# Optimization experiments

Hardware: AMD Instinct MI355X
Metric: run time of the kernel (lower is better)

Reference implementation:

```python
import jax, jax.numpy as jnp
import numpy as np

B, S, E, H = 2, 2048, 1024, 16
D = E // H  # head_dim = 64

def setup_inputs() -> dict:
    key = jax.random.key(0)
    ks = jax.random.split(key, 11)
    s = 1.0 / np.sqrt(E)
    inp = {
        'query': jax.random.normal(ks[0], (B, S, E), jnp.float32),
        'key':   jax.random.normal(ks[1], (B, S, E), jnp.float32),
        'value': jax.random.normal(ks[2], (B, S, E), jnp.float32),
        'Wq': jax.random.uniform(ks[3], (E, E), jnp.float32, -s, s),
        'bq': jax.random.uniform(ks[4], (E,), jnp.float32, -s, s),
        'Wk': jax.random.uniform(ks[5], (E, E), jnp.float32, -s, s),
        'bk': jax.random.uniform(ks[6], (E,), jnp.float32, -s, s),
        'Wv': jax.random.uniform(ks[7], (E, E), jnp.float32, -s, s),
        'bv': jax.random.uniform(ks[8], (E,), jnp.float32, -s, s),
        'Wo': jax.random.uniform(ks[9], (E, E), jnp.float32, -s, s),
        'bo': jax.random.uniform(ks[10], (E,), jnp.float32, -s, s),
    }
    return inp

def reference(query, key, value, Wq, bq, Wk, bk, Wv, bv, Wo, bo):
    # project and split heads: [B,S,E] -> [B,H,S,D]
    def proj(x, W, b):
        y = jnp.einsum('bse,fe->bsf', x, W) + b  # torch Linear: x @ W.T + b
        return y.reshape(B, S, H, D).transpose(0, 2, 1, 3)
    q = proj(query, Wq, bq)
    k = proj(key, Wk, bk)
    v = proj(value, Wv, bv)
    scores = jnp.einsum('bhqd,bhkd->bhqk', q, k) / jnp.sqrt(jnp.float32(D))
    attn = jax.nn.softmax(scores, axis=-1)
    out = jnp.einsum('bhqk,bhkd->bhqd', attn, v)  # [B,H,S,D]
    out = out.transpose(0, 2, 1, 3).reshape(B, S, E)
    return jnp.einsum('bse,fe->bsf', out, Wo) + bo
```

## Files before the change

### kernel.cpp

```cpp
#include <hip/hip_runtime.h>

#define B_ 2
#define S_ 2048
#define E_ 1024
#define H_ 16
#define D_ 64
#define M_ (B_*S_)
#define K_ E_

typedef __attribute__((ext_vector_type(8))) short  short8;
typedef __attribute__((ext_vector_type(4))) float  f32x4;
typedef __attribute__((ext_vector_type(8))) unsigned short u16x8;
typedef __attribute__((ext_vector_type(4))) unsigned short u16x4;
typedef __attribute__((ext_vector_type(4))) unsigned int   u32x4;

#define QSCALE 0.18033688011112042f

#if __has_builtin(__builtin_amdgcn_exp2f)
#define EXP2F(x) __builtin_amdgcn_exp2f(x)
#else
#define EXP2F(x) exp2f(x)
#endif

__device__ __forceinline__ unsigned short f2bf(float f) {
    unsigned u = __float_as_uint(f);
    u += 0x7fffu + ((u >> 16) & 1u);
    return (unsigned short)(u >> 16);
}

__device__ __forceinline__ void gl_lds16(const ushort* g, ushort* l) {
    __builtin_amdgcn_global_load_lds((const __attribute__((address_space(1))) void*)g,
                                     (__attribute__((address_space(3))) void*)l,
                                     16, 0, 0);
}

#define FL_SYNC(N) do {                                                   \
    asm volatile("s_waitcnt vmcnt(" #N ")" ::: "memory");                 \
    __builtin_amdgcn_s_barrier();                                         \
    asm volatile("" ::: "memory");                                        \
} while (0)

#define WAITL0_BAR() do {                                                 \
    asm volatile("s_waitcnt lgkmcnt(0)" ::: "memory");                    \
    __builtin_amdgcn_s_barrier();                                         \
    asm volatile("" ::: "memory");                                        \
} while (0)

__global__ __launch_bounds__(256)
void cvt_all(const float* __restrict__ q, const float* __restrict__ k,
             const float* __restrict__ v, const float* __restrict__ wq,
             const float* __restrict__ wk, const float* __restrict__ wv,
             const float* __restrict__ wo, ushort* __restrict__ dst)
{
    const int bid = blockIdx.x;
    const float* src;
    size_t dof;
    int local;
    if (bid < 6144) {
        const int t = bid >> 11;
        src = (t == 0) ? q : (t == 1) ? k : v;
        dof = (size_t)t * 4194304u;
        local = bid & 2047;
    } else {
        const int r = bid - 6144;
        const int t = r >> 9;
        src = (t == 0) ? wq : (t == 1) ? wk : (t == 2) ? wv : wo;
        dof = 12582912u + (size_t)t * 1048576u;
        local = r & 511;
    }
    const size_t idx = (size_t)local * 2048 + threadIdx.x * 8;
    const float4 a = *(const float4*)(src + idx);
    const float4 b = *(const float4*)(src + idx + 4);
    u16x8 o;
    o[0] = f2bf(a.x); o[1] = f2bf(a.y); o[2] = f2bf(a.z); o[3] = f2bf(a.w);
    o[4] = f2bf(b.x); o[5] = f2bf(b.y); o[6] = f2bf(b.z); o[7] = f2bf(b.w);
    *(u16x8*)(dst + dof + idx) = o;
}

template<int SWAP>
__device__ __forceinline__ void qkv_core(const ushort* __restrict__ X,
                                         const ushort* __restrict__ W,
                                         int m0, int n0,
                                         f32x4 acc[8][4], ushort* sh)
{
    const int tid  = threadIdx.x;
    const int lane = tid & 63;
    const int w    = tid >> 6;
    const int wm   = w & 1;
    const int wn   = w >> 1;
    const int l15  = lane & 15, quad = lane >> 4;

    const int srow = lane >> 3, schunk = lane & 7;
    const int scol = (schunk ^ srow) * 8;
    const ushort* pa[4]; const ushort* pb[4]; int loff[4];
    #pragma unroll
    for (int i = 0; i < 4; ++i) {
        const int row = (w * 4 + i) * 8 + srow;
        pa[i] = X + (size_t)(m0 + row) * K_ + scol;
        pb[i] = W + (size_t)(n0 + row) * K_ + scol;
        loff[i] = (w * 4 + i) * 512 + lane * 8;
    }

    const f32x4 zero = {0.f, 0.f, 0.f, 0.f};
    #pragma unroll
    for (int mt = 0; mt < 8; ++mt)
        #pragma unroll
        for (int nt = 0; nt < 4; ++nt) acc[mt][nt] = zero;

    #pragma unroll
    for (int i = 0; i < 4; ++i) {
        gl_lds16(pa[i],      sh + loff[i]);
        gl_lds16(pb[i],      sh + 16384 + loff[i]);
    }
    #pragma unroll
    for (int i = 0; i < 4; ++i) {
        gl_lds16(pa[i] + 64, sh + 32768 + loff[i]);
        gl_lds16(pb[i] + 64, sh + 32768 + 16384 + loff[i]);
    }

    const int arow = wm * 128 + l15;
    const int brow = wn * 64 + l15;

    for (int t = 0; t < 16; ++t) {
        ushort* curA = sh + (t & 1) * 32768;
        ushort* curB = curA + 16384;

        if (t < 15) { FL_SYNC(8); } else { FL_SYNC(0); }

        __builtin_amdgcn_s_setprio(1);
        #pragma unroll
        for (int kc = 0; kc < 2; ++kc) {
            short8 bf[4];
            #pragma unroll
            for (int nt = 0; nt < 4; ++nt) {
                const int r = brow + nt * 16;
                bf[nt] = *(const short8*)(curB + r * 64 + (((kc * 4 + quad) ^ (r & 7)) * 8));
            }
            #pragma unroll
            for (int mt = 0; mt < 8; ++mt) {
                const int r = arow + mt * 16;
                const short8 af = *(const short8*)(curA + r * 64 + (((kc * 4 + quad) ^ (r & 7)) * 8));
                #pragma unroll
                for (int nt = 0; nt < 4; ++nt) {
                    if (SWAP)
                        acc[mt][nt] = __builtin_amdgcn_mfma_f32_16x16x32_bf16(bf[nt], af, acc[mt][nt], 0, 0, 0);
                    else
                        acc[mt][nt] = __builtin_amdgcn_mfma_f32_16x16x32_bf16(af, bf[nt], acc[mt][nt], 0, 0, 0);
                }
            }
        }
        __builtin_amdgcn_s_setprio(0);

        if (t + 2 < 16) {
            WAITL0_BAR();
            const int k0 = (t + 2) * 64;
            #pragma unroll
            for (int i = 0; i < 4; ++i) {
                gl_lds16(pa[i] + k0, curA + loff[i]);
                gl_lds16(pb[i] + k0, curB + loff[i]);
            }
        }
    }
}

__global__ __launch_bounds__(512, 2)
void gemm_qkv(const ushort* __restrict__ Xq, const ushort* __restrict__ Xk,
              const ushort* __restrict__ Xv, const ushort* __restrict__ Wq,
              const ushort* __restrict__ Wk, const ushort* __restrict__ Wv,
              const float* __restrict__ bq, const float* __restrict__ bk,
              const float* __restrict__ bv, ushort* __restrict__ Qh,
              ushort* __restrict__ Kh, ushort* __restrict__ Vt)
{
    __shared__ ushort sh[65536];
    const int z = blockIdx.z;
    const ushort* X = (z == 0) ? Xq : (z == 1) ? Xk : Xv;
    const ushort* W = (z == 0) ? Wq : (z == 1) ? Wk : Wv;
    const float* bias = (z == 0) ? bq : (z == 1) ? bk : bv;
    ushort* dst = (z == 0) ? Qh : (z == 1) ? Kh : Vt;

    const int m0 = blockIdx.y * 256, n0 = blockIdx.x * 256;
    f32x4 acc[8][4];
    const int lane = threadIdx.x & 63, w = threadIdx.x >> 6;
    const int wm = w & 1, wn = w >> 1;
    const int l15 = lane & 15, quad = lane >> 4;

    if (z < 2) {
        qkv_core<1>(X, W, m0, n0, acc, sh);
        const float qsc = (z == 0) ? QSCALE : 1.0f;
        #pragma unroll
        for (int nt = 0; nt < 4; ++nt) {
            const int nb = n0 + wn * 64 + nt * 16 + quad * 4;
            const int h = nb >> 6, d0 = nb & 63;
            const float4 b4 = *(const float4*)(bias + nb);
            const float bb4[4] = {b4.x, b4.y, b4.z, b4.w};
            #pragma unroll
            for (int mt = 0; mt < 8; ++mt) {
                const int tok = m0 + wm * 128 + mt * 16 + l15;
                const int b = tok >> 11, s = tok & (S_ - 1);
                u16x4 pk;
                #pragma unroll
                for (int r = 0; r < 4; ++r)
                    pk[r] = f2bf((acc[mt][nt][r] + bb4[r]) * qsc);
                *(u16x4*)&dst[(((size_t)(b * H_ + h) * S_) + s) * D_ + d0] = pk;
            }
        }
    } else {
        qkv_core<0>(X, W, m0, n0, acc, sh);
        float bias4[4];
        #pragma unroll
        for (int nt = 0; nt < 4; ++nt)
            bias4[nt] = bias[n0 + wn * 64 + nt * 16 + l15];
        #pragma unroll
        for (int mt = 0; mt < 8; ++mt) {
            const int mrow0 = m0 + wm * 128 + mt * 16 + (quad * 4);
            const int b = mrow0 >> 11;
            const int s0 = mrow0 & (S_ - 1);
            #pragma unroll
            for (int nt = 0; nt < 4; ++nt) {
                const int n = n0 + wn * 64 + nt * 16 + l15;
                const int h = n >> 6, d = n & 63;
                u16x4 pk;
                #pragma unroll
                for (int r = 0; r < 4; ++r) pk[r] = f2bf(acc[mt][nt][r] + bias4[nt]);
                *(u16x4*)&Vt[(((size_t)(b * H_ + h) * D_) + d) * S_ + s0] = pk;
            }
        }
    }
}

__global__ __launch_bounds__(256)
void gemm_out(const ushort* __restrict__ X, const ushort* __restrict__ W,
              const float* __restrict__ bias, float* __restrict__ out)
{
    __shared__ ushort Ast[128 * 32];
    __shared__ ushort Bst[64 * 32];
    const int m0 = blockIdx.y * 128, n0 = blockIdx.x * 64;
    const int tid = threadIdx.x, lane = tid & 63, w = tid >> 6;
    const int wm = w & 1, wn = w >> 1;
    const int l15 = lane & 15, quad = lane >> 4;
    const int r0 = tid >> 2, c8 = (tid & 3) * 8;
    const int kb = quad * 8;

    const f32x4 zero = {0.f, 0.f, 0.f, 0.f};
    f32x4 acc[4][2];
    #pragma unroll
    for (int mt = 0; mt < 4; ++mt)
        #pragma unroll
        for (int nt = 0; nt < 2; ++nt) acc[mt][nt] = zero;

    for (int k0 = 0; k0 < K_; k0 += 32) {
        __syncthreads();
        const ushort* ga = X + (size_t)(m0 + r0) * K_ + k0 + c8;
        gl_lds16(ga, Ast + tid * 8);
        gl_lds16(ga + (size_t)64 * K_, Ast + 2048 + tid * 8);
        const ushort* gb = W + (size_t)(n0 + r0) * K_ + k0 + c8;
        gl_lds16(gb, Bst + tid * 8);
        __syncthreads();

        short8 af[4], bf[2];
        #pragma unroll
        for (int mt = 0; mt < 4; ++mt)
            af[mt] = *(const short8*)(Ast + (wm * 64 + mt * 16 + l15) * 32 + kb);
        #pragma unroll
        for (int nt = 0; nt < 2; ++nt)
            bf[nt] = *(const short8*)(Bst + (wn * 32 + nt * 16 + l15) * 32 + kb);
        #pragma unroll
        for (int mt = 0; mt < 4; ++mt)
            #pragma unroll
            for (int nt = 0; nt < 2; ++nt)
                acc[mt][nt] = __builtin_amdgcn_mfma_f32_16x16x32_bf16(af[mt], bf[nt], acc[mt][nt], 0, 0, 0);
    }

    float bias2[2];
    #pragma unroll
    for (int nt = 0; nt < 2; ++nt)
        bias2[nt] = bias[n0 + wn * 32 + nt * 16 + l15];

    #pragma unroll
    for (int mt = 0; mt < 4; ++mt) {
        const int mrow0 = m0 + wm * 64 + mt * 16 + quad * 4;
        #pragma unroll
        for (int nt = 0; nt < 2; ++nt) {
            const int n = n0 + wn * 32 + nt * 16 + l15;
            #pragma unroll
            for (int r = 0; r < 4; ++r)
                out[(size_t)(mrow0 + r) * E_ + n] = acc[mt][nt][r] + bias2[nt];
        }
    }
}

#define NTILE (S_ / 64)

__device__ __forceinline__ void flash_stage(const ushort* __restrict__ Kg,
                                            const ushort* __restrict__ Vg,
                                            size_t qk_off, size_t vt_off,
                                            ushort* sh, int j,
                                            int row0, int gcol0, int row1, int gcol1,
                                            int chunk0, int chunk1, int lane)
{
    ushort* sb = sh + 4096 + (j & 3) * 8192;
    const int j0n = j * 64;
    gl_lds16(Kg + qk_off + (size_t)(j0n + row0) * D_ + gcol0 * 8, sb + chunk0 * 512 + lane * 8);
    gl_lds16(Vg + vt_off + (size_t)row0 * S_ + j0n + gcol0 * 8, sb + 4096 + chunk0 * 512 + lane * 8);
    gl_lds16(Kg + qk_off + (size_t)(j0n + row1) * D_ + gcol1 * 8, sb + chunk1 * 512 + lane * 8);
    gl_lds16(Vg + vt_off + (size_t)row1 * S_ + j0n + gcol1 * 8, sb + 4096 + chunk1 * 512 + lane * 8);
}

__device__ __forceinline__ void flash_qk(const ushort* Kb, const ushort* Vb,
                                         const short8* qr0, const short8* qr1,
                                         int krow, int l15, int quad, int gidx,
                                         float* lsum, uint2* pout, uint2* vv)
{
    const short8 ka0 = *(const short8*)&Kb[krow + ((quad ^ (l15 & 7)) * 8)];
    const short8 ka1 = *(const short8*)&Kb[krow + (((4 + quad) ^ (l15 & 7)) * 8)];
    #pragma unroll
    for (int nt = 0; nt < 4; ++nt)
        vv[nt] = *(const uint2*)&Vb[(nt * 16 + l15) * 64 + gidx * 8 + (quad & 1) * 4];
    const f32x4 zero = {0.f, 0.f, 0.f, 0.f};
    #pragma unroll
    for (int g = 0; g < 4; ++g) {
        f32x4 t;
        t = __builtin_amdgcn_mfma_f32_16x16x32_bf16(ka0, qr0[g], zero, 0, 0, 0);
        t = __builtin_amdgcn_mfma_f32_16x16x32_bf16(ka1, qr1[g], t, 0, 0, 0);
        const float p0 = EXP2F(t[0]), p1 = EXP2F(t[1]);
        const float p2 = EXP2F(t[2]), p3 = EXP2F(t[3]);
        lsum[g] += (p0 + p1) + (p2 + p3);
        const unsigned a0 = __float_as_uint(p0) + 0x8000u;
        const unsigned a1 = __float_as_uint(p1) + 0x8000u;
        const unsigned a2 = __float_as_uint(p2) + 0x8000u;
        const unsigned a3 = __float_as_uint(p3) + 0x8000u;
        pout[g].x = (a1 & 0xffff0000u) | (a0 >> 16);
        pout[g].y = (a3 & 0xffff0000u) | (a2 >> 16);
    }
}

__device__ __forceinline__ void flash_pv(const uint2* paLo, const uint2* paHi,
                                         const uint2* vvA, const uint2* vvB,
                                         f32x4 o[4][4])
{
    short8 pa8[4];
    #pragma unroll
    for (int g = 0; g < 4; ++g) {
        u32x4 pk;
        pk[0] = paLo[g].x; pk[1] = paLo[g].y;
        pk[2] = paHi[g].x; pk[3] = paHi[g].y;
        pa8[g] = __builtin_bit_cast(short8, pk);
    }
    #pragma unroll
    for (int nt = 0; nt < 4; ++nt) {
        u32x4 vk;
        vk[0] = vvA[nt].x; vk[1] = vvA[nt].y;
        vk[2] = vvB[nt].x; vk[3] = vvB[nt].y;
        const short8 vb8 = __builtin_bit_cast(short8, vk);
        #pragma unroll
        for (int g = 0; g < 4; ++g)
            o[g][nt] = __builtin_amdgcn_mfma_f32_16x16x32_bf16(pa8[g], vb8, o[g][nt], 0, 0, 0);
    }
}

__global__ __launch_bounds__(256, 2)
void flash_mfma(const ushort* __restrict__ Qg, const ushort* __restrict__ Kg,
                const ushort* __restrict__ Vg, ushort* __restrict__ AO)
{
    __shared__ ushort sh[36864];
    ushort* Qs = sh;

    const int tid = threadIdx.x, lane = tid & 63, w = tid >> 6;
    const int l15 = lane & 15, quad = lane >> 4;
    const int q0 = blockIdx.x * 64, h = blockIdx.y, b = blockIdx.z;
    const size_t qk_off = (size_t)(b * H_ + h) * S_ * D_;
    const size_t vt_off = (size_t)(b * H_ + h) * D_ * S_;

    const int chunk0 = w, chunk1 = w + 4;
    const int row0 = chunk0 * 8 + (lane >> 3);
    const int row1 = chunk1 * 8 + (lane >> 3);
    const int gcol0 = (lane & 7) ^ (row0 & 7);
    const int gcol1 = (lane & 7) ^ (row1 & 7);

    gl_lds16(Qg + qk_off + (size_t)(q0 + row0) * D_ + gcol0 * 8, Qs + chunk0 * 512 + lane * 8);
    gl_lds16(Qg + qk_off + (size_t)(q0 + row1) * D_ + gcol1 * 8, Qs + chunk1 * 512 + lane * 8);
    flash_stage(Kg, Vg, qk_off, vt_off, sh, 0, row0, gcol0, row1, gcol1, chunk0, chunk1, lane);
    flash_stage(Kg, Vg, qk_off, vt_off, sh, 1, row0, gcol0, row1, gcol1, chunk0, chunk1, lane);
    flash_stage(Kg, Vg, qk_off, vt_off, sh, 2, row0, gcol0, row1, gcol1, chunk0, chunk1, lane);

    FL_SYNC(12);

    short8 qr0[4], qr1[4];
    #pragma unroll
    for (int g = 0; g < 4; ++g) {
        qr0[g] = *(const short8*)&Qs[(g * 16 + l15) * 64 + ((quad ^ (l15 & 7)) * 8)];
        qr1[g] = *(const short8*)&Qs[(g * 16 + l15) * 64 + (((4 + quad) ^ (l15 & 7)) * 8)];
    }

    const f32x4 zero = {0.f, 0.f, 0.f, 0.f};
    f32x4 o[4][4];
    #pragma unroll
    for (int g = 0; g < 4; ++g)
        #pragma unroll
        for (int nt = 0; nt < 4; ++nt) o[g][nt] = zero;
    float lsum[4] = {0.f, 0.f, 0.f, 0.f};

    const int krow = (w * 16 + l15) * 64;
    const int gidx = (2 * w + (quad >> 1)) ^ (l15 & 7);

    uint2 vvA[4], vvB[4], paLo[4], paHi[4];

    for (int p = 0; p < 15; ++p) {
        const int jA = 2 * p;
        FL_SYNC(8);
        flash_stage(Kg, Vg, qk_off, vt_off, sh, jA + 3,
                    row0, gcol0, row1, gcol1, chunk0, chunk1, lane);
        {
            const ushort* KbA = sh + 4096 + (jA & 3) * 8192;
            flash_qk(KbA, KbA + 4096, qr0, qr1, krow, l15, quad, gidx, lsum, paLo, vvA);
        }
        FL_SYNC(8);
        if (jA + 4 < NTILE)
            flash_stage(Kg, Vg, qk_off, vt_off, sh, jA + 4,
                        row0, gcol0, row1, gcol1, chunk0, chunk1, lane);
        {
            const ushort* KbB = sh + 4096 + ((jA + 1) & 3) * 8192;
            flash_qk(KbB, KbB + 4096, qr0, qr1, krow, l15, quad, gidx, lsum, paHi, vvB);
        }
        flash_pv(paLo, paHi, vvA, vvB, o);
    }

    FL_SYNC(4);
    {
        const ushort* KbA = sh + 4096 + (30 & 3) * 8192;
        flash_qk(KbA, KbA + 4096, qr0, qr1, krow, l15, quad, gidx, lsum, paLo, vvA);
    }
    FL_SYNC(0);
    {
        const ushort* KbB = sh + 4096 + (31 & 3) * 8192;
        flash_qk(KbB, KbB + 4096, qr0, qr1, krow, l15, quad, gidx, lsum, paHi, vvB);
    }
    flash_pv(paLo, paHi, vvA, vvB, o);

    #pragma unroll
    for (int g = 0; g < 4; ++g) {
        lsum[g] += __shfl_xor(lsum[g], 16);
        lsum[g] += __shfl_xor(lsum[g], 32);
    }
    __syncthreads();
    float* fb = (float*)sh;
    #pragma unroll
    for (int g = 0; g < 4; ++g) {
        if (w != g) {
            #pragma unroll
            for (int nt = 0; nt < 4; ++nt)
                #pragma unroll
                for (int r = 0; r < 4; ++r)
                    fb[w * 1024 + (nt * 4 + r) * 64 + lane] = o[g][nt][r];
            if (quad == 0) fb[4096 + w * 64 + l15] = lsum[g];
        }
        __syncthreads();
        if (w == g) {
            #pragma unroll
            for (int ws = 0; ws < 4; ++ws) {
                if (ws == g) continue;
                #pragma unroll
                for (int nt = 0; nt < 4; ++nt)
                    #pragma unroll
                    for (int r = 0; r < 4; ++r)
                        o[g][nt][r] += fb[ws * 1024 + (nt * 4 + r) * 64 + lane];
                lsum[g] += fb[4096 + ws * 64 + l15];
            }
        }
        __syncthreads();
    }

    #pragma unroll
    for (int g = 0; g < 4; ++g) {
        if (w == g) {
            const float inv = 1.0f / lsum[g];
            float invr[4];
            #pragma unroll
            for (int r = 0; r < 4; ++r)
                invr[r] = __shfl(inv, (lane & 0x30) | (quad * 4 + r));
            #pragma unroll
            for (int nt = 0; nt < 4; ++nt) {
                const int e = h * 64 + nt * 16 + l15;
                #pragma unroll
                for (int r = 0; r < 4; ++r) {
                    const int s = q0 + g * 16 + quad * 4 + r;
                    AO[(size_t)(b * S_ + s) * E_ + e] = f2bf(o[g][nt][r] * invr[r]);
                }
            }
        }
    }
}

extern "C" void kernel_launch(void* const* d_in, const int* in_sizes, int n_in,
                              void* d_out, int out_size, void* d_ws, size_t ws_size,
                              hipStream_t stream) {
    const float* query = (const float*)d_in[0];
    const float* key   = (const float*)d_in[1];
    const float* value = (const float*)d_in[2];
    const float* Wq = (const float*)d_in[3];
    const float* bq = (const float*)d_in[4];
    const float* Wk = (const float*)d_in[5];
    const float* bk = (const float*)d_in[6];
    const float* Wv = (const float*)d_in[7];
    const float* bv = (const float*)d_in[8];
    const float* Wo = (const float*)d_in[9];
    const float* bo = (const float*)d_in[10];
    float* out = (float*)d_out;

    ushort* ws = (ushort*)d_ws;
    ushort* Xq  = ws;
    ushort* Xk  = ws + 4194304u;
    ushort* Xv  = ws + 8388608u;
    ushort* Wqb = ws + 12582912u;
    ushort* Wkb = ws + 13631488u;
    ushort* Wvb = ws + 14680064u;
    ushort* Wob = ws + 15728640u;
    ushort* Qh  = ws + 16777216u;
    ushort* Kh  = ws + 20971520u;
    ushort* Vt  = ws + 25165824u;
    ushort* AO  = ws + 29360128u;

    cvt_all<<<8192, 256, 0, stream>>>(query, key, value, Wq, Wk, Wv, Wo, ws);
    gemm_qkv<<<dim3(4, 16, 3), 512, 0, stream>>>(Xq, Xk, Xv, Wqb, Wkb, Wvb,
                                                 bq, bk, bv, Qh, Kh, Vt);
    flash_mfma<<<dim3(32, 16, 2), 256, 0, stream>>>(Qh, Kh, Vt, AO);
    gemm_out<<<dim3(16, 32), 256, 0, stream>>>(AO, Wob, bo, out);
}
```

Before: 228.7 us.

## Shrink flash attention K/V ring to two LDS slots for higher occupancy

Cuts the K/V shared-memory ring from four slots to two, roughly halving the LDS footprint, and raises the launch-bounds occupancy hint from 2 to 4 blocks per CU. To keep the smaller ring safe, each tile's LDS values are now read into registers first, followed by a wait and barrier, before the async prefetch that overwrites that slot is issued. The goal is more resident waves to hide latency. The cost is a shallower prefetch distance and an extra barrier per tile, and the tighter register budget could cause spills.

```diff
diff --git a/kernel.cpp b/kernel.cpp
--- a/kernel.cpp
+++ b/kernel.cpp
@@ -298,7 +298,7 @@
                                             int row0, int gcol0, int row1, int gcol1,
                                             int chunk0, int chunk1, int lane)
 {
-    ushort* sb = sh + 4096 + (j & 3) * 8192;
+    ushort* sb = sh + 4096 + (j & 1) * 8192;
     const int j0n = j * 64;
     gl_lds16(Kg + qk_off + (size_t)(j0n + row0) * D_ + gcol0 * 8, sb + chunk0 * 512 + lane * 8);
     gl_lds16(Vg + vt_off + (size_t)row0 * S_ + j0n + gcol0 * 8, sb + 4096 + chunk0 * 512 + lane * 8);
@@ -306,22 +306,27 @@
     gl_lds16(Vg + vt_off + (size_t)row1 * S_ + j0n + gcol1 * 8, sb + 4096 + chunk1 * 512 + lane * 8);
 }
 
-__device__ __forceinline__ void flash_qk(const ushort* Kb, const ushort* Vb,
-                                         const short8* qr0, const short8* qr1,
-                                         int krow, int l15, int quad, int gidx,
-                                         float* lsum, uint2* pout, uint2* vv)
-{
-    const short8 ka0 = *(const short8*)&Kb[krow + ((quad ^ (l15 & 7)) * 8)];
-    const short8 ka1 = *(const short8*)&Kb[krow + (((4 + quad) ^ (l15 & 7)) * 8)];
+__device__ __forceinline__ void flash_ldsld(const ushort* Kb, const ushort* Vb,
+                                            int krow, int l15, int quad, int gidx,
+                                            short8* ka, uint2* vv)
+{
+    ka[0] = *(const short8*)&Kb[krow + ((quad ^ (l15 & 7)) * 8)];
+    ka[1] = *(const short8*)&Kb[krow + (((4 + quad) ^ (l15 & 7)) * 8)];
     #pragma unroll
     for (int nt = 0; nt < 4; ++nt)
         vv[nt] = *(const uint2*)&Vb[(nt * 16 + l15) * 64 + gidx * 8 + (quad & 1) * 4];
+}
+
+__device__ __forceinline__ void flash_qk(const short8* ka,
+                                         const short8* qr0, const short8* qr1,
+                                         float* lsum, uint2* pout)
+{
     const f32x4 zero = {0.f, 0.f, 0.f, 0.f};
     #pragma unroll
     for (int g = 0; g < 4; ++g) {
         f32x4 t;
-        t = __builtin_amdgcn_mfma_f32_16x16x32_bf16(ka0, qr0[g], zero, 0, 0, 0);
-        t = __builtin_amdgcn_mfma_f32_16x16x32_bf16(ka1, qr1[g], t, 0, 0, 0);
+        t = __builtin_amdgcn_mfma_f32_16x16x32_bf16(ka[0], qr0[g], zero, 0, 0, 0);
+        t = __builtin_amdgcn_mfma_f32_16x16x32_bf16(ka[1], qr1[g], t, 0, 0, 0);
         const float p0 = EXP2F(t[0]), p1 = EXP2F(t[1]);
         const float p2 = EXP2F(t[2]), p3 = EXP2F(t[3]);
         lsum[g] += (p0 + p1) + (p2 + p3);
@@ -358,11 +363,11 @@
     }
 }
 
-__global__ __launch_bounds__(256, 2)
+__global__ __launch_bounds__(256, 4)
 void flash_mfma(const ushort* __restrict__ Qg, const ushort* __restrict__ Kg,
                 const ushort* __restrict__ Vg, ushort* __restrict__ AO)
 {
-    __shared__ ushort sh[36864];
+    __shared__ ushort sh[20480];
     ushort* Qs = sh;
 
     const int tid = threadIdx.x, lane = tid & 63, w = tid >> 6;
@@ -381,9 +386,8 @@
     gl_lds16(Qg + qk_off + (size_t)(q0 + row1) * D_ + gcol1 * 8, Qs + chunk1 * 512 + lane * 8);
     flash_stage(Kg, Vg, qk_off, vt_off, sh, 0, row0, gcol0, row1, gcol1, chunk0, chunk1, lane);
     flash_stage(Kg, Vg, qk_off, vt_off, sh, 1, row0, gcol0, row1, gcol1, chunk0, chunk1, lane);
-    flash_stage(Kg, Vg, qk_off, vt_off, sh, 2, row0, gcol0, row1, gcol1, chunk0, chunk1, lane);
-
-    FL_SYNC(12);
+
+    FL_SYNC(8);
 
     short8 qr0[4], qr1[4];
     #pragma unroll
@@ -392,49 +396,44 @@
         qr1[g] = *(const short8*)&Qs[(g * 16 + l15) * 64 + (((4 + quad) ^ (l15 & 7)) * 8)];
     }
 
-    const f32x4 zero = {0.f, 0.f, 0.f, 0.f};
     f32x4 o[4][4];
     #pragma unroll
     for (int g = 0; g < 4; ++g)
         #pragma unroll
-        for (int nt = 0; nt < 4; ++nt) o[g][nt] = zero;
+        for (int nt = 0; nt < 4; ++nt) o[g][nt] = {0.f, 0.f, 0.f, 0.f};
     float lsum[4] = {0.f, 0.f, 0.f, 0.f};
 
     const int krow = (w * 16 + l15) * 64;
     const int gidx = (2 * w + (quad >> 1)) ^ (l15 & 7);
 
+    short8 ka[2];
     uint2 vvA[4], vvB[4], paLo[4], paHi[4];
+    const ushort* slot0 = sh + 4096;
+    const ushort* slot1 = sh + 4096 + 8192;
 
     for (int p = 0; p < 15; ++p) {
         const int jA = 2 * p;
-        FL_SYNC(8);
+        FL_SYNC(4);
+        flash_ldsld(slot0, slot0 + 4096, krow, l15, quad, gidx, ka, vvA);
+        WAITL0_BAR();
+        flash_stage(Kg, Vg, qk_off, vt_off, sh, jA + 2,
+                    row0, gcol0, row1, gcol1, chunk0, chunk1, lane);
+        flash_qk(ka, qr0, qr1, lsum, paLo);
+        FL_SYNC(4);
+        flash_ldsld(slot1, slot1 + 4096, krow, l15, quad, gidx, ka, vvB);
+        WAITL0_BAR();
         flash_stage(Kg, Vg, qk_off, vt_off, sh, jA + 3,
                     row0, gcol0, row1, gcol1, chunk0, chunk1, lane);
-        {
-            const ushort* KbA = sh + 4096 + (jA & 3) * 8192;
-            flash_qk(KbA, KbA + 4096, qr0, qr1, krow, l15, quad, gidx, lsum, paLo, vvA);
-        }
-        FL_SYNC(8);
-        if (jA + 4 < NTILE)
-            flash_stage(Kg, Vg, qk_off, vt_off, sh, jA + 4,
-                        row0, gcol0, row1, gcol1, chunk0, chunk1, lane);
-        {
-            const ushort* KbB = sh + 4096 + ((jA + 1) & 3) * 8192;
-            flash_qk(KbB, KbB + 4096, qr0, qr1, krow, l15, quad, gidx, lsum, paHi, vvB);
-        }
+        flash_qk(ka, qr0, qr1, lsum, paHi);
         flash_pv(paLo, paHi, vvA, vvB, o);
     }
 
     FL_SYNC(4);
-    {
-        const ushort* KbA = sh + 4096 + (30 & 3) * 8192;
-        flash_qk(KbA, KbA + 4096, qr0, qr1, krow, l15, quad, gidx, lsum, paLo, vvA);
-    }
+    flash_ldsld(slot0, slot0 + 4096, krow, l15, quad, gidx, ka, vvA);
+    flash_qk(ka, qr0, qr1, lsum, paLo);
     FL_SYNC(0);
-    {
-        const ushort* KbB = sh + 4096 + (31 & 3) * 8192;
-        flash_qk(KbB, KbB + 4096, qr0, qr1, krow, l15, quad, gidx, lsum, paHi, vvB);
-    }
+    flash_ldsld(slot1, slot1 + 4096, krow, l15, quad, gidx, ka, vvB);
+    flash_qk(ka, qr0, qr1, lsum, paHi);
     flash_pv(paLo, paHi, vvA, vvB, o);
 
     #pragma unroll
```

After: 470.5 us. 106% more time.
